# Optimization experiments

Measured on AMD Instinct MI355X. Metric: run time of the kernel, lower is better.

The kernel has to match this reference:

```python
import jax, jax.numpy as jnp
import numpy as np

B, S, E, H = 1, 2048, 1024, 16
D = E // H  # head_dim = 64


def setup_inputs() -> dict:
    key = jax.random.key(0)
    ks = jax.random.split(key, 9)
    sd = 0.02
    hidden_states = jax.random.normal(ks[0], (B, S, E), dtype=jnp.float32)
    # causal mask: positions with mask==0 are filled with -inf (per masked_fill_)
    mask = jnp.tril(jnp.ones((1, 1, S, S), dtype=bool))
    Wq = jax.random.normal(ks[1], (E, E), dtype=jnp.float32) * sd
    bq = jax.random.normal(ks[2], (E,), dtype=jnp.float32) * sd
    Wk = jax.random.normal(ks[3], (D, E), dtype=jnp.float32) * sd
    bk = jax.random.normal(ks[4], (D,), dtype=jnp.float32) * sd
    Wv = jax.random.normal(ks[5], (D, E), dtype=jnp.float32) * sd
    bv = jax.random.normal(ks[6], (D,), dtype=jnp.float32) * sd
    Wo = jax.random.normal(ks[7], (E, E), dtype=jnp.float32) * sd
    bo = jax.random.normal(ks[8], (E,), dtype=jnp.float32) * sd
    return {"hidden_states": hidden_states, "mask": mask,
            "Wq": Wq, "bq": bq, "Wk": Wk, "bk": bk,
            "Wv": Wv, "bv": bv, "Wo": Wo, "bo": bo}


def reference(hidden_states, mask, Wq, bq, Wk, bk, Wv, bv, Wo, bo):
    bsz, tgt_len, embed_dim = hidden_states.shape
    # projections (torch Linear: x @ W^T + b)
    q = hidden_states @ Wq.T + bq                       # [B, S, E]
    q = q.reshape(bsz, tgt_len, H, D).transpose(0, 2, 1, 3)  # [B, H, S, D]
    k = hidden_states @ Wk.T + bk                       # [B, S, D] shared single KV head
    v = hidden_states @ Wv.T + bv                       # [B, S, D]
    scaling = jnp.sqrt(jnp.asarray(D, dtype=hidden_states.dtype))
    # QK^T with implicit broadcast of the shared K head (instead of expand)
    scores = jnp.einsum('bhqd,bkd->bhqk', q, k) / scaling   # [B, H, S, S]
    scores = jnp.where(mask, scores, -jnp.inf)
    probs = jax.nn.softmax(scores, axis=-1)             # dropout p=0 -> identity
    attn = jnp.einsum('bhqk,bkd->bhqd', probs, v)       # [B, H, S, D]
    attn = attn.transpose(0, 2, 1, 3).reshape(bsz, tgt_len, H * D)
    return attn @ Wo.T + bo                             # [B, S, E]
```

## Files before the change

kernel.cpp:

```cpp
#include <hip/hip_runtime.h>
#include <hip/hip_bf16.h>

typedef __hip_bfloat16 bf16;
typedef __attribute__((ext_vector_type(8))) short short8;
typedef __attribute__((ext_vector_type(4))) float f32x4;

__device__ __forceinline__ short8 ld8(const void* p) { return *(const short8*)p; }

__device__ __forceinline__ void async_cp16(bf16* lds, const bf16* g) {
    __builtin_amdgcn_global_load_lds(
        (const __attribute__((address_space(1))) unsigned int*)g,
        (__attribute__((address_space(3))) unsigned int*)lds, 16, 0, 0);
}

struct bf4 { bf16 a, b, c, d; };

__global__ void cast_kernel(const float* __restrict__ s0, bf16* __restrict__ d0, int n0_,
                            const float* __restrict__ s1, bf16* __restrict__ d1, int n1_,
                            const float* __restrict__ s2, bf16* __restrict__ d2, int n2_,
                            const float* __restrict__ s3, bf16* __restrict__ d3, int n3_,
                            const float* __restrict__ s4, bf16* __restrict__ d4, int n4_) {
    const float* srcs[5] = {s0, s1, s2, s3, s4};
    bf16* dsts[5] = {d0, d1, d2, d3, d4};
    int ns[5] = {n0_, n1_, n2_, n3_, n4_};
    int stride = gridDim.x * blockDim.x;
    int t0 = blockIdx.x * blockDim.x + threadIdx.x;
#pragma unroll
    for (int a = 0; a < 5; ++a) {
        const float4* src = (const float4*)srcs[a];
        bf4* dst = (bf4*)dsts[a];
        int n4 = ns[a] >> 2;
        for (int i = t0; i < n4; i += stride) {
            float4 v = src[i];
            bf4 o = {__float2bfloat16(v.x), __float2bfloat16(v.y),
                     __float2bfloat16(v.z), __float2bfloat16(v.w)};
            dst[i] = o;
        }
    }
}

#define GEMM_STAGE(dst, src_base, row0, ldk)                                   \
    _Pragma("unroll")                                                          \
    for (int u = 0; u < 4; ++u) {                                              \
        int t = wave * 4 + u;                                                  \
        int row = t * 4 + (lane >> 4);                                         \
        int gsrc = (lane & 15) ^ (row & 15);                                   \
        async_cp16(&dst[t * 4][0], src_base + (size_t)(row0 + row) * ldk + k0 + gsrc * 8); \
    }

__global__ void qkv_proj_kernel(const bf16* __restrict__ A,
                                const bf16* __restrict__ Wq, const bf16* __restrict__ Wk,
                                const bf16* __restrict__ Wv,
                                const float* __restrict__ bq, const float* __restrict__ bk,
                                const float* __restrict__ bv,
                                bf16* __restrict__ qo, bf16* __restrict__ ko,
                                bf16* __restrict__ vto, int M, int K) {
    __shared__ __align__(16) bf16 As[64][128];
    __shared__ __align__(16) bf16 Bs[64][128];
    const int nt = blockIdx.x;
    const bf16* W;
    const float* bias;
    int mode, nw0;
    if (nt < 16)      { W = Wq; bias = bq; mode = 0; nw0 = nt * 64; }
    else if (nt == 16){ W = Wk; bias = bk; mode = 1; nw0 = 0; }
    else              { W = Wv; bias = bv; mode = 2; nw0 = 0; }

    const int tid = threadIdx.x;
    const int wave = tid >> 6, lane = tid & 63;
    const int l16 = lane & 15, quad = lane >> 4;
    const int wr = wave >> 1, wc = wave & 1;
    const int m0 = blockIdx.y * 64;

    f32x4 acc[2][2];
    const f32x4 z = {0.f, 0.f, 0.f, 0.f};
#pragma unroll
    for (int mi = 0; mi < 2; ++mi)
#pragma unroll
        for (int ni = 0; ni < 2; ++ni) acc[mi][ni] = z;

    for (int k0 = 0; k0 < K; k0 += 128) {
        GEMM_STAGE(As, A, m0, K)
        GEMM_STAGE(Bs, W, nw0, K)
        __syncthreads();

        short8 af[2][4], bfr[2][4];
#pragma unroll
        for (int mi = 0; mi < 2; ++mi) {
            int R = wr * 32 + mi * 16 + l16;
#pragma unroll
            for (int kc = 0; kc < 4; ++kc)
                af[mi][kc] = ld8(&As[R][((kc * 4 + quad) ^ (R & 15)) * 8]);
        }
#pragma unroll
        for (int ni = 0; ni < 2; ++ni) {
            int r = wc * 32 + ni * 16 + l16;
#pragma unroll
            for (int kc = 0; kc < 4; ++kc)
                bfr[ni][kc] = ld8(&Bs[r][((kc * 4 + quad) ^ (r & 15)) * 8]);
        }
#pragma unroll
        for (int kc = 0; kc < 4; ++kc)
#pragma unroll
            for (int mi = 0; mi < 2; ++mi)
#pragma unroll
                for (int ni = 0; ni < 2; ++ni)
                    acc[mi][ni] = __builtin_amdgcn_mfma_f32_16x16x32_bf16(
                        af[mi][kc], bfr[ni][kc], acc[mi][ni], 0, 0, 0);
        __syncthreads();
    }

#pragma unroll
    for (int mi = 0; mi < 2; ++mi)
#pragma unroll
        for (int ni = 0; ni < 2; ++ni)
#pragma unroll
            for (int r = 0; r < 4; ++r) {
                int row = m0 + wr * 32 + mi * 16 + quad * 4 + r;
                int c = wc * 32 + ni * 16 + l16;
                float v = acc[mi][ni][r] + bias[nw0 + c];
                if (mode == 0)
                    qo[(size_t)row * 1024 + nt * 64 + c] = __float2bfloat16(v * 0.125f);
                else if (mode == 1)
                    ko[(size_t)row * 64 + c] = __float2bfloat16(v);
                else
                    vto[(size_t)c * M + row] = __float2bfloat16(v);
            }
}

__global__ void gemm_bt_mfma(const bf16* __restrict__ A, const bf16* __restrict__ W,
                             const float* __restrict__ bias, float* __restrict__ C,
                             int M, int N, int K) {
    __shared__ __align__(16) bf16 As[64][128];
    __shared__ __align__(16) bf16 Bs[64][128];
    const int tid = threadIdx.x;
    const int wave = tid >> 6, lane = tid & 63;
    const int l16 = lane & 15, quad = lane >> 4;
    const int wr = wave >> 1, wc = wave & 1;
    const int m0 = blockIdx.y * 64, n0 = blockIdx.x * 64;

    f32x4 acc[2][2];
    const f32x4 z = {0.f, 0.f, 0.f, 0.f};
#pragma unroll
    for (int mi = 0; mi < 2; ++mi)
#pragma unroll
        for (int ni = 0; ni < 2; ++ni) acc[mi][ni] = z;

    for (int k0 = 0; k0 < K; k0 += 128) {
        GEMM_STAGE(As, A, m0, K)
        GEMM_STAGE(Bs, W, n0, K)
        __syncthreads();

        short8 af[2][4], bfr[2][4];
#pragma unroll
        for (int mi = 0; mi < 2; ++mi) {
            int R = wr * 32 + mi * 16 + l16;
#pragma unroll
            for (int kc = 0; kc < 4; ++kc)
                af[mi][kc] = ld8(&As[R][((kc * 4 + quad) ^ (R & 15)) * 8]);
        }
#pragma unroll
        for (int ni = 0; ni < 2; ++ni) {
            int r = wc * 32 + ni * 16 + l16;
#pragma unroll
            for (int kc = 0; kc < 4; ++kc)
                bfr[ni][kc] = ld8(&Bs[r][((kc * 4 + quad) ^ (r & 15)) * 8]);
        }
#pragma unroll
        for (int kc = 0; kc < 4; ++kc)
#pragma unroll
            for (int mi = 0; mi < 2; ++mi)
#pragma unroll
                for (int ni = 0; ni < 2; ++ni)
                    acc[mi][ni] = __builtin_amdgcn_mfma_f32_16x16x32_bf16(
                        af[mi][kc], bfr[ni][kc], acc[mi][ni], 0, 0, 0);
        __syncthreads();
    }

#pragma unroll
    for (int mi = 0; mi < 2; ++mi)
#pragma unroll
        for (int ni = 0; ni < 2; ++ni)
#pragma unroll
            for (int r = 0; r < 4; ++r) {
                int row = m0 + wr * 32 + mi * 16 + quad * 4 + r;
                int col = n0 + wc * 32 + ni * 16 + l16;
                C[(size_t)row * N + col] = acc[mi][ni][r] + bias[col];
            }
}

__global__ void flash_mfma_kernel(const bf16* __restrict__ Q, const bf16* __restrict__ Kg,
                                  const bf16* __restrict__ VT,
                                  bf16* __restrict__ Opart, float* __restrict__ Lpart,
                                  bf16* __restrict__ attn, int S) {
    const int s = blockIdx.x;
    int i, c;
    if (s < 32)      { c = 0; i = s; }
    else if (s < 56) { c = 1; i = s - 24; }
    else if (s < 72) { c = 2; i = s - 40; }
    else             { c = 3; i = s - 48; }

    __shared__ __align__(16) bf16 Ks[2][64][64];
    __shared__ __align__(16) bf16 Vt[2][64][64];
    __shared__ bf16 Ps[4][16][68];

    const int h = blockIdx.y;
    const int q0 = i * 64;
    const int tid = threadIdx.x;
    const int wave = tid >> 6, lane = tid & 63;
    const int l16 = lane & 15, quad = lane >> 4;
    const int lr = lane >> 3, lsw = (lane & 7) ^ (lr & 7);
    const int qrow = q0 + wave * 16;

    short8 qf[2];
#pragma unroll
    for (int kc = 0; kc < 2; ++kc)
        qf[kc] = ld8(Q + (size_t)(qrow + l16) * 1024 + h * 64 + kc * 32 + quad * 8);

    short8 onesf;
    {
        short o = (l16 == 0) ? (short)0x3F80 : (short)0;
        onesf[0]=o; onesf[1]=o; onesf[2]=o; onesf[3]=o;
        onesf[4]=o; onesf[5]=o; onesf[6]=o; onesf[7]=o;
    }

    f32x4 of[4];
    const f32x4 z = {0.f, 0.f, 0.f, 0.f};
#pragma unroll
    for (int dt = 0; dt < 4; ++dt) of[dt] = z;
    f32x4 lacc = z;

    const int jt0 = c * 8;
    const int jt1 = min(c * 8 + 8, i + 1);
    const int nits = jt1 - jt0;

#define STAGE_KV(buf, jt_)                                                       \
    do {                                                                         \
        const int j0_ = (jt_) * 64;                                              \
        _Pragma("unroll")                                                        \
        for (int u = 0; u < 2; ++u) {                                            \
            int t = wave * 2 + u;                                                \
            async_cp16(&Ks[buf][t * 8][0],                                       \
                       Kg + (size_t)(j0_ + t * 8 + lr) * 64 + lsw * 8);          \
            async_cp16(&Vt[buf][t * 8][0],                                       \
                       VT + (size_t)(t * 8 + lr) * S + j0_ + lsw * 8);           \
        }                                                                        \
    } while (0)

    STAGE_KV(0, jt0);
    __syncthreads();

    for (int it = 0; it < nits; ++it) {
        const int jt = jt0 + it;
        const int j0 = jt * 64;
        const int cur = it & 1;
        if (it + 1 < nits) STAGE_KV(cur ^ 1, jt + 1);

        f32x4 sc[4];
#pragma unroll
        for (int nt = 0; nt < 4; ++nt) {
            int R = nt * 16 + l16;
            sc[nt] = __builtin_amdgcn_mfma_f32_16x16x32_bf16(
                qf[0], ld8(&Ks[cur][R][(quad ^ (R & 7)) * 8]), z, 0, 0, 0);
            sc[nt] = __builtin_amdgcn_mfma_f32_16x16x32_bf16(
                qf[1], ld8(&Ks[cur][R][((4 + quad) ^ (R & 7)) * 8]), sc[nt], 0, 0, 0);
        }
        bool need_mask = (j0 + 63 > qrow);
        if (need_mask) {
#pragma unroll
            for (int nt = 0; nt < 4; ++nt)
#pragma unroll
                for (int r = 0; r < 4; ++r)
                    if (j0 + nt * 16 + l16 > qrow + quad * 4 + r) sc[nt][r] = -1e30f;
        }

#pragma unroll
        for (int nt = 0; nt < 4; ++nt)
#pragma unroll
            for (int r = 0; r < 4; ++r)
                Ps[wave][quad * 4 + r][nt * 16 + l16] = __float2bfloat16(__expf(sc[nt][r]));

        short8 pf[2];
        pf[0] = ld8(&Ps[wave][l16][quad * 8]);
        pf[1] = ld8(&Ps[wave][l16][32 + quad * 8]);

        lacc = __builtin_amdgcn_mfma_f32_16x16x32_bf16(pf[0], onesf, lacc, 0, 0, 0);
        lacc = __builtin_amdgcn_mfma_f32_16x16x32_bf16(pf[1], onesf, lacc, 0, 0, 0);

#pragma unroll
        for (int dt = 0; dt < 4; ++dt) {
            int R = dt * 16 + l16;
            of[dt] = __builtin_amdgcn_mfma_f32_16x16x32_bf16(
                pf[0], ld8(&Vt[cur][R][(quad ^ (R & 7)) * 8]), of[dt], 0, 0, 0);
            of[dt] = __builtin_amdgcn_mfma_f32_16x16x32_bf16(
                pf[1], ld8(&Vt[cur][R][((4 + quad) ^ (R & 7)) * 8]), of[dt], 0, 0, 0);
        }
        __syncthreads();
    }
#undef STAGE_KV

    if (s < 8) {
        float inv[4];
#pragma unroll
        for (int r = 0; r < 4; ++r)
            inv[r] = 1.f / __shfl(lacc[r], quad * 16);
#pragma unroll
        for (int dt = 0; dt < 4; ++dt)
#pragma unroll
            for (int r = 0; r < 4; ++r) {
                int row = q0 + wave * 16 + quad * 4 + r;
                attn[(size_t)row * 1024 + h * 64 + dt * 16 + l16] =
                    __float2bfloat16(of[dt][r] * inv[r]);
            }
        return;
    }

    bf16* Op = Opart + ((size_t)s * 16 + h) * 4096;
#pragma unroll
    for (int dt = 0; dt < 4; ++dt)
#pragma unroll
        for (int r = 0; r < 4; ++r) {
            int row = wave * 16 + quad * 4 + r;
            Op[row * 64 + dt * 16 + l16] = __float2bfloat16(of[dt][r]);
        }
    if (l16 == 0) {
        float* L = Lpart + ((size_t)s * 16 + h) * 64;
#pragma unroll
        for (int r = 0; r < 4; ++r)
            L[wave * 16 + quad * 4 + r] = lacc[r];
    }
}

__global__ void flash_merge_kernel(const bf16* __restrict__ Opart,
                                   const float* __restrict__ Lpart,
                                   bf16* __restrict__ attn) {
    const int i = blockIdx.x + 8, h = blockIdx.y;
    const int nch = (i >> 3) + 1;
    const int tid = threadIdx.x;
    const int row = tid >> 2, cg = (tid & 3) * 16;

    float L = 0.f;
    for (int cc = 0; cc < nch; ++cc) {
        int s = (cc == 0) ? i : (cc == 1) ? 24 + i : (cc == 2) ? 40 + i : 48 + i;
        L += Lpart[((size_t)s * 16 + h) * 64 + row];
    }
    float inv = 1.f / L;

    float o[16];
#pragma unroll
    for (int j = 0; j < 16; ++j) o[j] = 0.f;
    for (int cc = 0; cc < nch; ++cc) {
        int s = (cc == 0) ? i : (cc == 1) ? 24 + i : (cc == 2) ? 40 + i : 48 + i;
        const bf16* Op = Opart + ((size_t)s * 16 + h) * 4096 + row * 64 + cg;
#pragma unroll
        for (int j = 0; j < 16; ++j) o[j] += __bfloat162float(Op[j]);
    }
    bf16* dst = attn + (size_t)(i * 64 + row) * 1024 + h * 64 + cg;
#pragma unroll
    for (int j = 0; j < 16; ++j) dst[j] = __float2bfloat16(o[j] * inv);
}

extern "C" void kernel_launch(void* const* d_in, const int* in_sizes, int n_in,
                              void* d_out, int out_size, void* d_ws, size_t ws_size,
                              hipStream_t stream) {
    const int S = 2048, E = 1024, D = 64;

    const float* hs = (const float*)d_in[0];
    const float* Wq = (const float*)d_in[2];
    const float* bq = (const float*)d_in[3];
    const float* Wk = (const float*)d_in[4];
    const float* bk = (const float*)d_in[5];
    const float* Wv = (const float*)d_in[6];
    const float* bv = (const float*)d_in[7];
    const float* Wo = (const float*)d_in[8];
    const float* bo = (const float*)d_in[9];
    float* out = (float*)d_out;

    bf16* ws = (bf16*)d_ws;
    bf16* hsb = ws;
    bf16* wqb = hsb + (size_t)S * E;
    bf16* wkb = wqb + (size_t)E * E;
    bf16* wvb = wkb + (size_t)D * E;
    bf16* wob = wvb + (size_t)D * E;
    bf16* q = wob + (size_t)E * E;
    bf16* kbuf = q + (size_t)S * E;
    bf16* vt = kbuf + (size_t)S * D;
    bf16* attn = vt + (size_t)S * D;
    bf16* Opart = attn + (size_t)S * E;
    float* Lpart = (float*)(Opart + (size_t)1280 * 4096);

    cast_kernel<<<512, 256, 0, stream>>>(hs, hsb, S * E,
                                         Wq, wqb, E * E,
                                         Wk, wkb, D * E,
                                         Wv, wvb, D * E,
                                         Wo, wob, E * E);
    qkv_proj_kernel<<<dim3(18, S / 64), 256, 0, stream>>>(hsb, wqb, wkb, wvb,
                                                          bq, bk, bv,
                                                          q, kbuf, vt, S, E);
    flash_mfma_kernel<<<dim3(80, 16), 256, 0, stream>>>(q, kbuf, vt, Opart, Lpart, attn, S);
    flash_merge_kernel<<<dim3(24, 16), 256, 0, stream>>>(Opart, Lpart, attn);
    gemm_bt_mfma<<<dim3(E / 64, S / 64), 256, 0, stream>>>(attn, wob, bo, out, S, E, E);
}
```

Before: 148.3 us.

## Double-buffer GEMM tile staging and single-buffer attention KV tiles

Both projection GEMMs (QKV and output) get two LDS buffers per operand, so the next K-slice is fetched asynchronously while the current one feeds the MFMAs, hiding global-load latency. The attention kernel goes the other way: its K/V tiles drop from double to single buffering, with a load and barrier at the top of each iteration. That cuts attention LDS use, which may raise occupancy, but the load latency is no longer overlapped there. GEMM LDS use doubles to 64KB per block, which may lower occupancy.

```diff
diff --git a/kernel.cpp b/kernel.cpp
--- a/kernel.cpp
+++ b/kernel.cpp
@@ -39,14 +39,16 @@
     }
 }
 
-#define GEMM_STAGE(dst, src_base, row0, ldk)                                   \
-    _Pragma("unroll")                                                          \
-    for (int u = 0; u < 4; ++u) {                                              \
-        int t = wave * 4 + u;                                                  \
-        int row = t * 4 + (lane >> 4);                                         \
-        int gsrc = (lane & 15) ^ (row & 15);                                   \
-        async_cp16(&dst[t * 4][0], src_base + (size_t)(row0 + row) * ldk + k0 + gsrc * 8); \
-    }
+__device__ __forceinline__ void stage64(bf16 (*dst)[128], const bf16* src,
+                                        int ldk, int k0, int wave, int lane) {
+#pragma unroll
+    for (int u = 0; u < 4; ++u) {
+        int t = wave * 4 + u;
+        int row = t * 4 + (lane >> 4);
+        int gsrc = (lane & 15) ^ (row & 15);
+        async_cp16(&dst[t * 4][0], src + (size_t)row * ldk + k0 + gsrc * 8);
+    }
+}
 
 __global__ void qkv_proj_kernel(const bf16* __restrict__ A,
                                 const bf16* __restrict__ Wq, const bf16* __restrict__ Wk,
@@ -55,8 +57,8 @@
                                 const float* __restrict__ bv,
                                 bf16* __restrict__ qo, bf16* __restrict__ ko,
                                 bf16* __restrict__ vto, int M, int K) {
-    __shared__ __align__(16) bf16 As[64][128];
-    __shared__ __align__(16) bf16 Bs[64][128];
+    __shared__ __align__(16) bf16 As[2][64][128];
+    __shared__ __align__(16) bf16 Bs[2][64][128];
     const int nt = blockIdx.x;
     const bf16* W;
     const float* bias;
@@ -70,6 +72,8 @@
     const int l16 = lane & 15, quad = lane >> 4;
     const int wr = wave >> 1, wc = wave & 1;
     const int m0 = blockIdx.y * 64;
+    const bf16* Abase = A + (size_t)m0 * K;
+    const bf16* Wbase = W + (size_t)nw0 * K;
 
     f32x4 acc[2][2];
     const f32x4 z = {0.f, 0.f, 0.f, 0.f};
@@ -78,25 +82,31 @@
 #pragma unroll
         for (int ni = 0; ni < 2; ++ni) acc[mi][ni] = z;
 
-    for (int k0 = 0; k0 < K; k0 += 128) {
-        GEMM_STAGE(As, A, m0, K)
-        GEMM_STAGE(Bs, W, nw0, K)
-        __syncthreads();
-
+    const int nk = K / 128;
+    stage64(As[0], Abase, K, 0, wave, lane);
+    stage64(Bs[0], Wbase, K, 0, wave, lane);
+    __syncthreads();
+
+    for (int kt = 0; kt < nk; ++kt) {
+        const int cur = kt & 1;
+        if (kt + 1 < nk) {
+            stage64(As[cur ^ 1], Abase, K, (kt + 1) * 128, wave, lane);
+            stage64(Bs[cur ^ 1], Wbase, K, (kt + 1) * 128, wave, lane);
+        }
         short8 af[2][4], bfr[2][4];
 #pragma unroll
         for (int mi = 0; mi < 2; ++mi) {
             int R = wr * 32 + mi * 16 + l16;
 #pragma unroll
             for (int kc = 0; kc < 4; ++kc)
-                af[mi][kc] = ld8(&As[R][((kc * 4 + quad) ^ (R & 15)) * 8]);
+                af[mi][kc] = ld8(&As[cur][R][((kc * 4 + quad) ^ (R & 15)) * 8]);
         }
 #pragma unroll
         for (int ni = 0; ni < 2; ++ni) {
             int r = wc * 32 + ni * 16 + l16;
 #pragma unroll
             for (int kc = 0; kc < 4; ++kc)
-                bfr[ni][kc] = ld8(&Bs[r][((kc * 4 + quad) ^ (r & 15)) * 8]);
+                bfr[ni][kc] = ld8(&Bs[cur][r][((kc * 4 + quad) ^ (r & 15)) * 8]);
         }
 #pragma unroll
         for (int kc = 0; kc < 4; ++kc)
@@ -130,13 +140,15 @@
 __global__ void gemm_bt_mfma(const bf16* __restrict__ A, const bf16* __restrict__ W,
                              const float* __restrict__ bias, float* __restrict__ C,
                              int M, int N, int K) {
-    __shared__ __align__(16) bf16 As[64][128];
-    __shared__ __align__(16) bf16 Bs[64][128];
+    __shared__ __align__(16) bf16 As[2][64][128];
+    __shared__ __align__(16) bf16 Bs[2][64][128];
     const int tid = threadIdx.x;
     const int wave = tid >> 6, lane = tid & 63;
     const int l16 = lane & 15, quad = lane >> 4;
     const int wr = wave >> 1, wc = wave & 1;
     const int m0 = blockIdx.y * 64, n0 = blockIdx.x * 64;
+    const bf16* Abase = A + (size_t)m0 * K;
+    const bf16* Wbase = W + (size_t)n0 * K;
 
     f32x4 acc[2][2];
     const f32x4 z = {0.f, 0.f, 0.f, 0.f};
@@ -145,25 +157,31 @@
 #pragma unroll
         for (int ni = 0; ni < 2; ++ni) acc[mi][ni] = z;
 
-    for (int k0 = 0; k0 < K; k0 += 128) {
-        GEMM_STAGE(As, A, m0, K)
-        GEMM_STAGE(Bs, W, n0, K)
-        __syncthreads();
-
+    const int nk = K / 128;
+    stage64(As[0], Abase, K, 0, wave, lane);
+    stage64(Bs[0], Wbase, K, 0, wave, lane);
+    __syncthreads();
+
+    for (int kt = 0; kt < nk; ++kt) {
+        const int cur = kt & 1;
+        if (kt + 1 < nk) {
+            stage64(As[cur ^ 1], Abase, K, (kt + 1) * 128, wave, lane);
+            stage64(Bs[cur ^ 1], Wbase, K, (kt + 1) * 128, wave, lane);
+        }
         short8 af[2][4], bfr[2][4];
 #pragma unroll
         for (int mi = 0; mi < 2; ++mi) {
             int R = wr * 32 + mi * 16 + l16;
 #pragma unroll
             for (int kc = 0; kc < 4; ++kc)
-                af[mi][kc] = ld8(&As[R][((kc * 4 + quad) ^ (R & 15)) * 8]);
+                af[mi][kc] = ld8(&As[cur][R][((kc * 4 + quad) ^ (R & 15)) * 8]);
         }
 #pragma unroll
         for (int ni = 0; ni < 2; ++ni) {
             int r = wc * 32 + ni * 16 + l16;
 #pragma unroll
             for (int kc = 0; kc < 4; ++kc)
-                bfr[ni][kc] = ld8(&Bs[r][((kc * 4 + quad) ^ (r & 15)) * 8]);
+                bfr[ni][kc] = ld8(&Bs[cur][r][((kc * 4 + quad) ^ (r & 15)) * 8]);
         }
 #pragma unroll
         for (int kc = 0; kc < 4; ++kc)
@@ -199,8 +217,8 @@
     else if (s < 72) { c = 2; i = s - 40; }
     else             { c = 3; i = s - 48; }
 
-    __shared__ __align__(16) bf16 Ks[2][64][64];
-    __shared__ __align__(16) bf16 Vt[2][64][64];
+    __shared__ __align__(16) bf16 Ks[64][64];
+    __shared__ __align__(16) bf16 Vt[64][64];
     __shared__ bf16 Ps[4][16][68];
 
     const int h = blockIdx.y;
@@ -231,38 +249,25 @@
 
     const int jt0 = c * 8;
     const int jt1 = min(c * 8 + 8, i + 1);
-    const int nits = jt1 - jt0;
-
-#define STAGE_KV(buf, jt_)                                                       \
-    do {                                                                         \
-        const int j0_ = (jt_) * 64;                                              \
-        _Pragma("unroll")                                                        \
-        for (int u = 0; u < 2; ++u) {                                            \
-            int t = wave * 2 + u;                                                \
-            async_cp16(&Ks[buf][t * 8][0],                                       \
-                       Kg + (size_t)(j0_ + t * 8 + lr) * 64 + lsw * 8);          \
-            async_cp16(&Vt[buf][t * 8][0],                                       \
-                       VT + (size_t)(t * 8 + lr) * S + j0_ + lsw * 8);           \
-        }                                                                        \
-    } while (0)
-
-    STAGE_KV(0, jt0);
-    __syncthreads();
-
-    for (int it = 0; it < nits; ++it) {
-        const int jt = jt0 + it;
+
+    for (int jt = jt0; jt < jt1; ++jt) {
         const int j0 = jt * 64;
-        const int cur = it & 1;
-        if (it + 1 < nits) STAGE_KV(cur ^ 1, jt + 1);
+#pragma unroll
+        for (int u = 0; u < 2; ++u) {
+            int t = wave * 2 + u;
+            async_cp16(&Ks[t * 8][0], Kg + (size_t)(j0 + t * 8 + lr) * 64 + lsw * 8);
+            async_cp16(&Vt[t * 8][0], VT + (size_t)(t * 8 + lr) * S + j0 + lsw * 8);
+        }
+        __syncthreads();
 
         f32x4 sc[4];
 #pragma unroll
         for (int nt = 0; nt < 4; ++nt) {
             int R = nt * 16 + l16;
             sc[nt] = __builtin_amdgcn_mfma_f32_16x16x32_bf16(
-                qf[0], ld8(&Ks[cur][R][(quad ^ (R & 7)) * 8]), z, 0, 0, 0);
+                qf[0], ld8(&Ks[R][(quad ^ (R & 7)) * 8]), z, 0, 0, 0);
             sc[nt] = __builtin_amdgcn_mfma_f32_16x16x32_bf16(
-                qf[1], ld8(&Ks[cur][R][((4 + quad) ^ (R & 7)) * 8]), sc[nt], 0, 0, 0);
+                qf[1], ld8(&Ks[R][((4 + quad) ^ (R & 7)) * 8]), sc[nt], 0, 0, 0);
         }
         bool need_mask = (j0 + 63 > qrow);
         if (need_mask) {
@@ -290,13 +295,12 @@
         for (int dt = 0; dt < 4; ++dt) {
             int R = dt * 16 + l16;
             of[dt] = __builtin_amdgcn_mfma_f32_16x16x32_bf16(
-                pf[0], ld8(&Vt[cur][R][(quad ^ (R & 7)) * 8]), of[dt], 0, 0, 0);
+                pf[0], ld8(&Vt[R][(quad ^ (R & 7)) * 8]), of[dt], 0, 0, 0);
             of[dt] = __builtin_amdgcn_mfma_f32_16x16x32_bf16(
-                pf[1], ld8(&Vt[cur][R][((4 + quad) ^ (R & 7)) * 8]), of[dt], 0, 0, 0);
+                pf[1], ld8(&Vt[R][((4 + quad) ^ (R & 7)) * 8]), of[dt], 0, 0, 0);
         }
         __syncthreads();
     }
-#undef STAGE_KV
 
     if (s < 8) {
         float inv[4];
```

Measured after the change: 151.7 us. +2.3%, slower.

## Keep P in registers via transposed QK^T and drop LDS round-trip and ones-MFMA

Applied to the files above, without the earlier changes.

Swaps the MFMA operand order for QK^T so the score accumulator layout directly matches the A-operand layout of 16x16x16 bf16 MFMAs, letting P feed the PV product from registers instead of going through a shared-memory Ps buffer. The row sum is computed with scalar adds plus cross-lane shuffles rather than an extra MFMA against a ones vector. It also removes double buffering of K/V, loading each tile synchronously before compute, which cuts LDS use but exposes global load latency each iteration. PV now uses twice as many smaller MFMAs with 8-byte LDS reads.

```diff
diff --git a/kernel.cpp b/kernel.cpp
--- a/kernel.cpp
+++ b/kernel.cpp
@@ -3,9 +3,11 @@
 
 typedef __hip_bfloat16 bf16;
 typedef __attribute__((ext_vector_type(8))) short short8;
+typedef __attribute__((ext_vector_type(4))) short short4v;
 typedef __attribute__((ext_vector_type(4))) float f32x4;
 
 __device__ __forceinline__ short8 ld8(const void* p) { return *(const short8*)p; }
+__device__ __forceinline__ short4v ld4(const void* p) { return *(const short4v*)p; }
 
 __device__ __forceinline__ void async_cp16(bf16* lds, const bf16* g) {
     __builtin_amdgcn_global_load_lds(
@@ -199,9 +201,8 @@
     else if (s < 72) { c = 2; i = s - 40; }
     else             { c = 3; i = s - 48; }
 
-    __shared__ __align__(16) bf16 Ks[2][64][64];
-    __shared__ __align__(16) bf16 Vt[2][64][64];
-    __shared__ bf16 Ps[4][16][68];
+    __shared__ __align__(16) bf16 Ks[64][64];
+    __shared__ __align__(16) bf16 Vt[64][64];
 
     const int h = blockIdx.y;
     const int q0 = i * 64;
@@ -216,93 +217,76 @@
     for (int kc = 0; kc < 2; ++kc)
         qf[kc] = ld8(Q + (size_t)(qrow + l16) * 1024 + h * 64 + kc * 32 + quad * 8);
 
-    short8 onesf;
-    {
-        short o = (l16 == 0) ? (short)0x3F80 : (short)0;
-        onesf[0]=o; onesf[1]=o; onesf[2]=o; onesf[3]=o;
-        onesf[4]=o; onesf[5]=o; onesf[6]=o; onesf[7]=o;
-    }
-
     f32x4 of[4];
     const f32x4 z = {0.f, 0.f, 0.f, 0.f};
 #pragma unroll
     for (int dt = 0; dt < 4; ++dt) of[dt] = z;
-    f32x4 lacc = z;
+    float lsum = 0.f;
 
     const int jt0 = c * 8;
     const int jt1 = min(c * 8 + 8, i + 1);
-    const int nits = jt1 - jt0;
-
-#define STAGE_KV(buf, jt_)                                                       \
-    do {                                                                         \
-        const int j0_ = (jt_) * 64;                                              \
-        _Pragma("unroll")                                                        \
-        for (int u = 0; u < 2; ++u) {                                            \
-            int t = wave * 2 + u;                                                \
-            async_cp16(&Ks[buf][t * 8][0],                                       \
-                       Kg + (size_t)(j0_ + t * 8 + lr) * 64 + lsw * 8);          \
-            async_cp16(&Vt[buf][t * 8][0],                                       \
-                       VT + (size_t)(t * 8 + lr) * S + j0_ + lsw * 8);           \
-        }                                                                        \
-    } while (0)
-
-    STAGE_KV(0, jt0);
-    __syncthreads();
-
-    for (int it = 0; it < nits; ++it) {
-        const int jt = jt0 + it;
+
+    for (int jt = jt0; jt < jt1; ++jt) {
         const int j0 = jt * 64;
-        const int cur = it & 1;
-        if (it + 1 < nits) STAGE_KV(cur ^ 1, jt + 1);
+#pragma unroll
+        for (int u = 0; u < 2; ++u) {
+            int t = wave * 2 + u;
+            async_cp16(&Ks[t * 8][0], Kg + (size_t)(j0 + t * 8 + lr) * 64 + lsw * 8);
+            async_cp16(&Vt[t * 8][0], VT + (size_t)(t * 8 + lr) * S + j0 + lsw * 8);
+        }
+        __syncthreads();
 
         f32x4 sc[4];
 #pragma unroll
         for (int nt = 0; nt < 4; ++nt) {
             int R = nt * 16 + l16;
             sc[nt] = __builtin_amdgcn_mfma_f32_16x16x32_bf16(
-                qf[0], ld8(&Ks[cur][R][(quad ^ (R & 7)) * 8]), z, 0, 0, 0);
+                ld8(&Ks[R][(quad ^ (R & 7)) * 8]), qf[0], z, 0, 0, 0);
             sc[nt] = __builtin_amdgcn_mfma_f32_16x16x32_bf16(
-                qf[1], ld8(&Ks[cur][R][((4 + quad) ^ (R & 7)) * 8]), sc[nt], 0, 0, 0);
-        }
-        bool need_mask = (j0 + 63 > qrow);
-        if (need_mask) {
+                ld8(&Ks[R][((4 + quad) ^ (R & 7)) * 8]), qf[1], sc[nt], 0, 0, 0);
+        }
+        if (j0 + 63 > qrow) {
 #pragma unroll
             for (int nt = 0; nt < 4; ++nt)
 #pragma unroll
                 for (int r = 0; r < 4; ++r)
-                    if (j0 + nt * 16 + l16 > qrow + quad * 4 + r) sc[nt][r] = -1e30f;
-        }
-
+                    if (j0 + nt * 16 + quad * 4 + r > qrow + l16) sc[nt][r] = -1e30f;
+        }
+
+        short4v p4[4];
 #pragma unroll
         for (int nt = 0; nt < 4; ++nt)
 #pragma unroll
-            for (int r = 0; r < 4; ++r)
-                Ps[wave][quad * 4 + r][nt * 16 + l16] = __float2bfloat16(__expf(sc[nt][r]));
-
-        short8 pf[2];
-        pf[0] = ld8(&Ps[wave][l16][quad * 8]);
-        pf[1] = ld8(&Ps[wave][l16][32 + quad * 8]);
-
-        lacc = __builtin_amdgcn_mfma_f32_16x16x32_bf16(pf[0], onesf, lacc, 0, 0, 0);
-        lacc = __builtin_amdgcn_mfma_f32_16x16x32_bf16(pf[1], onesf, lacc, 0, 0, 0);
+            for (int r = 0; r < 4; ++r) {
+                bf16 b = __float2bfloat16(__expf(sc[nt][r]));
+                lsum += __bfloat162float(b);
+                p4[nt][r] = *reinterpret_cast<short*>(&b);
+            }
 
 #pragma unroll
         for (int dt = 0; dt < 4; ++dt) {
-            int R = dt * 16 + l16;
-            of[dt] = __builtin_amdgcn_mfma_f32_16x16x32_bf16(
-                pf[0], ld8(&Vt[cur][R][(quad ^ (R & 7)) * 8]), of[dt], 0, 0, 0);
-            of[dt] = __builtin_amdgcn_mfma_f32_16x16x32_bf16(
-                pf[1], ld8(&Vt[cur][R][((4 + quad) ^ (R & 7)) * 8]), of[dt], 0, 0, 0);
-        }
-        __syncthreads();
-    }
-#undef STAGE_KV
+            int d = dt * 16 + l16;
+            int xr = d & 7;
+#pragma unroll
+            for (int nt = 0; nt < 4; ++nt) {
+                int g = 2 * nt + (quad >> 1);
+                short4v vf = ld4(&Vt[d][((g ^ xr) * 8) + (quad & 1) * 4]);
+                of[dt] = __builtin_amdgcn_mfma_f32_16x16x16bf16_1k(
+                    p4[nt], vf, of[dt], 0, 0, 0);
+            }
+        }
+        __syncthreads();
+    }
+
+    float Lred = lsum;
+    Lred += __shfl_xor(Lred, 16);
+    Lred += __shfl_xor(Lred, 32);
 
     if (s < 8) {
         float inv[4];
 #pragma unroll
         for (int r = 0; r < 4; ++r)
-            inv[r] = 1.f / __shfl(lacc[r], quad * 16);
+            inv[r] = 1.f / __shfl(Lred, quad * 4 + r);
 #pragma unroll
         for (int dt = 0; dt < 4; ++dt)
 #pragma unroll
@@ -322,11 +306,9 @@
             int row = wave * 16 + quad * 4 + r;
             Op[row * 64 + dt * 16 + l16] = __float2bfloat16(of[dt][r]);
         }
-    if (l16 == 0) {
+    if (quad == 0) {
         float* L = Lpart + ((size_t)s * 16 + h) * 64;
-#pragma unroll
-        for (int r = 0; r < 4; ++r)
-            L[wave * 16 + quad * 4 + r] = lacc[r];
+        L[wave * 16 + l16] = Lred;
     }
 }
 
```

Measured after the change: 138.8 us. -6.4%, faster.
